# Kernel tuning notes

Hardware: AMD Instinct MI355X
Metric: run time of the kernel (lower is better)

## Reference

```python
import jax, jax.numpy as jnp
import numpy as np

DIM = 128
HEADS = 8
DH = DIM // HEADS
WIN = (4, 4, 4)
TOPK = 4
EPS = 1e-6


def _ln(x, g, b):
    mu = jnp.mean(x, -1, keepdims=True)
    var = jnp.mean((x - mu) ** 2, -1, keepdims=True)
    return (x - mu) * jax.lax.rsqrt(var + EPS) * g + b


def _win3d(x, p1, p2, p3):
    # x: [B,S,H,W,C] -> [B, p1*p2*p3, Ms, Mh, Mw, C]
    B, S, H, W, C = x.shape
    Ms, Mh, Mw = S // p1, H // p2, W // p3
    x = x.reshape(B, p1, Ms, p2, Mh, p3, Mw, C)
    x = x.transpose(0, 1, 3, 5, 2, 4, 6, 7)
    return x.reshape(B, p1 * p2 * p3, Ms, Mh, Mw, C)


def setup_inputs() -> dict:
    key = jax.random.key(0)
    ks = jax.random.split(key, 20)

    def lin(k, din, dout):
        return jax.random.normal(k, (din, dout), jnp.float32) * 0.02

    return {
        "x_in": jax.random.normal(ks[0], (2, 128, 16, 32, 32), jnp.float32),
        "x_g_in": jax.random.normal(ks[1], (2, 128, 8, 16, 16), jnp.float32),
        # Atten (global branch)
        "qkv_w": lin(ks[2], DIM, 3 * DIM), "qkv_b": jnp.zeros((3 * DIM,), jnp.float32),
        "proj_w": lin(ks[3], DIM, DIM), "proj_b": jnp.zeros((DIM,), jnp.float32),
        # shared LayerNorm (self.norm1 is reused everywhere in the original)
        "ln_g": jnp.ones((DIM,), jnp.float32), "ln_b": jnp.zeros((DIM,), jnp.float32),
        # mlp (global branch FFN)
        "mlp_w1": lin(ks[4], DIM, 4 * DIM), "mlp_b1": jnp.zeros((4 * DIM,), jnp.float32),
        "mlp_w2": lin(ks[5], 4 * DIM, DIM), "mlp_b2": jnp.zeros((DIM,), jnp.float32),
        # TopkRouting
        "rq_w": lin(ks[6], DIM, DIM), "rq_b": jnp.zeros((DIM,), jnp.float32),
        "rk_w": lin(ks[7], DIM, DIM), "rk_b": jnp.zeros((DIM,), jnp.float32),
        # fused qkv over concatenated local+gathered-global tokens
        "gqkv_w": lin(ks[8], DIM, 3 * DIM), "gqkv_b": jnp.zeros((3 * DIM,), jnp.float32),
        "wo_w": lin(ks[9], DIM, DIM), "wo_b": jnp.zeros((DIM,), jnp.float32),
        # mlp2 (local branch FFN)
        "mlp2_w1": lin(ks[10], DIM, 4 * DIM), "mlp2_b1": jnp.zeros((4 * DIM,), jnp.float32),
        "mlp2_w2": lin(ks[11], 4 * DIM, DIM), "mlp2_b2": jnp.zeros((DIM,), jnp.float32),
    }


def reference(x_in, x_g_in, qkv_w, qkv_b, proj_w, proj_b, ln_g, ln_b,
              mlp_w1, mlp_b1, mlp_w2, mlp_b2, rq_w, rq_b, rk_w, rk_b,
              gqkv_w, gqkv_b, wo_w, wo_b, mlp2_w1, mlp2_b1, mlp2_w2, mlp2_b2):
    B, C, S, H, W = x_in.shape
    Ms, Mh, Mw = WIN
    p1, p2, p3 = S // Ms, H // Mh, W // Mw  # pads are zero for these shapes
    nw, w3l = p1 * p2 * p3, Ms * Mh * Mw
    scale = DIM ** -0.5  # BiLevelRoutingAttention.scale = dim**-0.5 (not per-head)

    x = jnp.transpose(x_in, (0, 2, 3, 4, 1))  # [B,S,H,W,C]
    shortcut_l = _win3d(x, p1, p2, p3).reshape(B, nw, w3l, C)

    # ---- global branch: full self-attention + FFN ----
    _, _, gS, gH, gW = x_g_in.shape
    gN = gS * gH * gW
    xg = jnp.transpose(x_g_in, (0, 2, 3, 4, 1)).reshape(B, gN, C)
    h = _ln(xg, ln_g, ln_b)
    qkv = (h @ qkv_w + qkv_b).reshape(B, gN, 3, HEADS, DH).transpose(2, 0, 3, 1, 4)
    q, k, v = qkv[0], qkv[1], qkv[2]
    a = jax.nn.softmax(jnp.einsum('bhnd,bhmd->bhnm', q, k) * DH ** -0.5, axis=-1)
    o = jnp.einsum('bhnm,bhmd->bhnd', a, v).transpose(0, 2, 1, 3).reshape(B, gN, C)
    xg = (o @ proj_w + proj_b) + xg
    xg4 = xg.reshape(B, gS, gH, gW, C)
    h = _ln(xg4, ln_g, ln_b)
    xg4 = xg4 + (jax.nn.gelu(h @ mlp_w1 + mlp_b1, approximate=False) @ mlp_w2 + mlp_b2)

    # ---- top-k window routing ----
    swg = _win3d(xg4, p1, p2, p3)  # [B,nw,gMs,gMh,gMw,C]
    w3g = swg.shape[2] * swg.shape[3] * swg.shape[4]
    g_win = swg.mean((2, 3, 4))  # [B,nw,C]
    qh = g_win @ rq_w + rq_b
    kh = g_win @ rk_w + rk_b
    logit = jnp.einsum('bnc,bmc->bnm', qh * scale, kh)
    _tvals, tidx = jax.lax.top_k(logit, TOPK)  # r_weight is computed but unused in the original forward

    # gather top-k global windows' tokens per local window
    gflat = swg.reshape(B, nw, w3g, C)
    gath = jax.vmap(lambda kv, idx: kv[idx])(gflat, tidx)  # [B,nw,topk,w3g,C]
    sc = jnp.concatenate([shortcut_l, gath.reshape(B, nw, TOPK * w3g, C)], axis=2)
    w3 = w3l + TOPK * w3g

    # ---- local+routed attention over concatenated tokens ----
    qkvp = _ln(sc, ln_g, ln_b) @ gqkv_w + gqkv_b
    qp, kp, vp = jnp.split(qkvp, 3, axis=-1)
    qp = qp.reshape(B, nw, w3, HEADS, DH)
    kp = kp.reshape(B, nw, w3, HEADS, DH)
    vp = vp.reshape(B, nw, w3, HEADS, DH)
    aw = jax.nn.softmax(jnp.einsum('bnqhd,bnkhd->bnhqk', qp * scale, kp), axis=-1)
    out = jnp.einsum('bnhqk,bnkhd->bnqhd', aw, vp).reshape(B, nw, w3, C)

    l = out[:, :, :w3l] @ wo_w + wo_b + shortcut_l
    l = l.reshape(B, p1, p2, p3, Ms, Mh, Mw, C).transpose(0, 1, 4, 2, 5, 3, 6, 7).reshape(B, S, H, W, C)
    l = l + (jax.nn.gelu(_ln(l, ln_g, ln_b) @ mlp2_w1 + mlp2_b1, approximate=False) @ mlp2_w2 + mlp2_b2)

    l_out = jnp.transpose(l, (0, 4, 1, 2, 3))
    g_out = jnp.transpose(xg4, (0, 4, 1, 2, 3))
    return (l_out, g_out)
```

## Files before the change

### kernel.cpp

```cpp
#include <hip/hip_runtime.h>
#include <hip/hip_bf16.h>
#include <math.h>

#define BATCH 2
#define CDIM 128
#define SS 16
#define HH_ 32
#define WW_ 32
#define NSP (SS*HH_*WW_)
#define GS 8
#define GH 16
#define GW 16
#define GN (GS*GH*GW)
#define HEADS 8
#define DH 16
#define NW 256
#define W3L 64
#define W3G 8
#define TOPK 4
#define W3 (W3L + TOPK*W3G)
#define LN_EPS 1e-6f
#define ROUTE_SCALE 0.08838834764831845f
#define GATTN_SCALE 0.25f

typedef short bshort8 __attribute__((ext_vector_type(8)));
typedef float f32x4 __attribute__((ext_vector_type(4)));

__device__ __forceinline__ unsigned short f2bf(float f) {
    unsigned int u = __float_as_uint(f);
    unsigned int r = (u + 0x7fffu + ((u >> 16) & 1u)) >> 16;
    return (unsigned short)r;
}
__device__ __forceinline__ float bf2f_lo(unsigned int u) { return __uint_as_float(u << 16); }
__device__ __forceinline__ float bf2f_hi(unsigned int u) { return __uint_as_float(u & 0xffff0000u); }

__device__ __forceinline__ float gelu_exact(float x) {
    return 0.5f * x * (1.0f + erff(x * 0.70710678118654752f));
}

__device__ __forceinline__ float shfl_sum32(float v) {
#pragma unroll
    for (int m = 16; m > 0; m >>= 1) v += __shfl_xor(v, m);
    return v;
}
__device__ __forceinline__ float shfl_sum16(float v) {
#pragma unroll
    for (int m = 8; m > 0; m >>= 1) v += __shfl_xor(v, m);
    return v;
}
__device__ __forceinline__ float shfl_sum8(float v) {
#pragma unroll
    for (int m = 4; m > 0; m >>= 1) v += __shfl_xor(v, m);
    return v;
}

__global__ __launch_bounds__(256) void k_wprep_all(const float* __restrict__ gqkv_w,
        const float* __restrict__ m2_w1, const float* __restrict__ m2_w2,
        const float* __restrict__ proj_w, const float* __restrict__ mlp_w1,
        const float* __restrict__ mlp_w2, const float* __restrict__ wo_w,
        unsigned short* __restrict__ wt, unsigned short* __restrict__ w1t,
        unsigned short* __restrict__ w2t, unsigned short* __restrict__ projt,
        unsigned short* __restrict__ gw1t, unsigned short* __restrict__ gw2t,
        unsigned short* __restrict__ wot) {
    int id = blockIdx.x * 256 + threadIdx.x;
    if (id < 49152) {
        int n = id >> 7, k = id & 127;
        float v = gqkv_w[k * 384 + n];
        if (n < 128) v *= ROUTE_SCALE;
        wt[id] = f2bf(v);
    } else if (id < 114688) {
        int i = id - 49152; int n = i >> 7, k = i & 127;
        w1t[i] = f2bf(m2_w1[k * 512 + n]);
    } else if (id < 180224) {
        int i = id - 114688; int n = i >> 9, k = i & 511;
        w2t[i] = f2bf(m2_w2[k * 128 + n]);
    } else if (id < 196608) {
        int i = id - 180224; int n = i >> 7, k = i & 127;
        projt[i] = f2bf(proj_w[k * 128 + n]);
    } else if (id < 262144) {
        int i = id - 196608; int n = i >> 7, k = i & 127;
        gw1t[i] = f2bf(mlp_w1[k * 512 + n]);
    } else if (id < 327680) {
        int i = id - 262144; int n = i >> 9, k = i & 511;
        gw2t[i] = f2bf(mlp_w2[k * 128 + n]);
    } else {
        int i = id - 327680; int n = i >> 7, k = i & 127;
        wot[i] = f2bf(wo_w[k * 128 + n]);
    }
}

__global__ __launch_bounds__(256) void k_gqkv2(const float* __restrict__ xg_in,
        const float* __restrict__ qkv_w, const float* __restrict__ qkv_b,
        const float* __restrict__ ln_g, const float* __restrict__ ln_b,
        float* __restrict__ xg, unsigned short* __restrict__ qgb,
        unsigned short* __restrict__ kgb, unsigned short* __restrict__ vgtb) {
    int blk = blockIdx.x; int b = blk >> 8; int n0 = (blk & 255) * 8;
    int t = threadIdx.x;
    __shared__ float xs[8][128];
    __shared__ float h[8][128];
    {
        int c = t >> 1, q4 = (t & 1) * 4;
        float4 v = *(const float4*)(xg_in + ((size_t)(b * 128 + c)) * GN + n0 + q4);
        xs[q4 + 0][c] = v.x; xs[q4 + 1][c] = v.y; xs[q4 + 2][c] = v.z; xs[q4 + 3][c] = v.w;
    }
    __syncthreads();
    int j = t >> 5, c4 = (t & 31) * 4;
    float4 v = *(float4*)&xs[j][c4];
    *(float4*)(xg + ((size_t)(b * GN) + n0 + j) * 128 + c4) = v;
    float s1 = shfl_sum32(v.x + v.y + v.z + v.w);
    float mu = s1 * (1.0f / 128.0f);
    float d0 = v.x - mu, d1 = v.y - mu, d2 = v.z - mu, d3 = v.w - mu;
    float s2 = shfl_sum32(d0 * d0 + d1 * d1 + d2 * d2 + d3 * d3);
    float rs = rsqrtf(s2 * (1.0f / 128.0f) + LN_EPS);
    float4 g4 = *(const float4*)(ln_g + c4);
    float4 b4 = *(const float4*)(ln_b + c4);
    float4 hn = { d0 * rs * g4.x + b4.x, d1 * rs * g4.y + b4.y,
                  d2 * rs * g4.z + b4.z, d3 * rs * g4.w + b4.w };
    *(float4*)&h[j][c4] = hn;
    __syncthreads();
    for (int c = t; c < 384; c += 256) {
        float acc[8];
        float bias = qkv_b[c];
#pragma unroll
        for (int jj = 0; jj < 8; jj++) acc[jj] = bias;
        for (int k = 0; k < 128; k++) {
            float w = qkv_w[k * 384 + c];
#pragma unroll
            for (int jj = 0; jj < 8; jj++) acc[jj] = fmaf(h[jj][k], w, acc[jj]);
        }
        int part = c >> 7, head = (c >> 4) & 7, d = c & 15;
        int bh = b * HEADS + head;
        if (part == 0) {
#pragma unroll
            for (int jj = 0; jj < 8; jj++)
                qgb[((size_t)bh * GN + n0 + jj) * DH + d] = f2bf(acc[jj] * GATTN_SCALE);
        } else if (part == 1) {
#pragma unroll
            for (int jj = 0; jj < 8; jj++)
                kgb[((size_t)bh * GN + n0 + jj) * DH + d] = f2bf(acc[jj]);
        } else {
            ushort4 u0, u1;
            u0.x = f2bf(acc[0]); u0.y = f2bf(acc[1]); u0.z = f2bf(acc[2]); u0.w = f2bf(acc[3]);
            u1.x = f2bf(acc[4]); u1.y = f2bf(acc[5]); u1.z = f2bf(acc[6]); u1.w = f2bf(acc[7]);
            unsigned short* dst = vgtb + ((size_t)bh * DH + d) * GN + n0;
            *(ushort4*)dst = u0; *(ushort4*)(dst + 4) = u1;
        }
    }
}

__global__ __launch_bounds__(256) void k_gattn_mfma(const unsigned short* __restrict__ qgb,
        const unsigned short* __restrict__ kgb, const unsigned short* __restrict__ vgtb,
        float* __restrict__ og) {
    int blk = blockIdx.x;
    int bh = blk >> 7; int qt = (blk & 127) << 4;
    int b = bh >> 3, hh = bh & 7;
    int t = threadIdx.x; int w = t >> 6; int lane = t & 63;
    int col = lane & 15, quad = lane >> 4;
    __shared__ __align__(16) unsigned short Pbuf[4 * 16 * 40];
    __shared__ float po[4][64][4];
    __shared__ float pl[4][64][4];

    bshort8 aq = {0, 0, 0, 0, 0, 0, 0, 0};
    if (quad < 2)
        aq = *(const bshort8*)(qgb + ((size_t)bh * GN + qt + col) * DH + quad * 8);

    f32x4 o = {0.f, 0.f, 0.f, 0.f};
    float lsum[4] = {0.f, 0.f, 0.f, 0.f};
    const unsigned short* kb = kgb + (size_t)bh * GN * DH;
    const unsigned short* vb = vgtb + (size_t)bh * DH * GN;
    unsigned short* pb = Pbuf + w * (16 * 40);
    int row0 = quad * 4;
    int kbeg = w * 512;
    for (int kc = kbeg; kc < kbeg + 512; kc += 32) {
        bshort8 bk0 = {0, 0, 0, 0, 0, 0, 0, 0};
        bshort8 bk1 = {0, 0, 0, 0, 0, 0, 0, 0};
        if (quad < 2) {
            bk0 = *(const bshort8*)(kb + (size_t)(kc + col) * DH + quad * 8);
            bk1 = *(const bshort8*)(kb + (size_t)(kc + 16 + col) * DH + quad * 8);
        }
        f32x4 z = {0.f, 0.f, 0.f, 0.f};
        f32x4 s0 = __builtin_amdgcn_mfma_f32_16x16x32_bf16(aq, bk0, z, 0, 0, 0);
        f32x4 s1 = __builtin_amdgcn_mfma_f32_16x16x32_bf16(aq, bk1, z, 0, 0, 0);
        float p0[4], p1[4];
#pragma unroll
        for (int r = 0; r < 4; r++) {
            p0[r] = __expf(s0[r]); p1[r] = __expf(s1[r]);
            lsum[r] += p0[r] + p1[r];
        }
#pragma unroll
        for (int r = 0; r < 4; r++) {
            pb[(row0 + r) * 40 + col] = f2bf(p0[r]);
            pb[(row0 + r) * 40 + 16 + col] = f2bf(p1[r]);
        }
        bshort8 pA = *(const bshort8*)(pb + col * 40 + quad * 8);
        bshort8 bv = *(const bshort8*)(vb + (size_t)col * GN + kc + quad * 8);
        o = __builtin_amdgcn_mfma_f32_16x16x32_bf16(pA, bv, o, 0, 0, 0);
    }
#pragma unroll
    for (int r = 0; r < 4; r++) {
        float v = lsum[r];
        v += __shfl_xor(v, 1); v += __shfl_xor(v, 2);
        v += __shfl_xor(v, 4); v += __shfl_xor(v, 8);
        lsum[r] = v;
    }
#pragma unroll
    for (int r = 0; r < 4; r++) { po[w][lane][r] = o[r]; pl[w][lane][r] = lsum[r]; }
    __syncthreads();
    if (w == 0) {
#pragma unroll
        for (int r = 0; r < 4; r++) {
            float os = po[0][lane][r] + po[1][lane][r] + po[2][lane][r] + po[3][lane][r];
            float ls = pl[0][lane][r] + pl[1][lane][r] + pl[2][lane][r] + pl[3][lane][r];
            og[((size_t)(b * GN) + qt + quad * 4 + r) * 128 + hh * 16 + col] = os / ls;
        }
    }
}

__global__ __launch_bounds__(256) void k_gmlp_mfma(const float* __restrict__ og,
        const float* __restrict__ xg,
        const unsigned short* __restrict__ projt, const float* __restrict__ proj_b,
        const float* __restrict__ ln_g, const float* __restrict__ ln_b,
        const unsigned short* __restrict__ gw1t, const float* __restrict__ b1,
        const unsigned short* __restrict__ gw2t, const float* __restrict__ b2,
        float* __restrict__ xg4, float* __restrict__ gout) {
    int blk = blockIdx.x; int b = blk >> 7; int n0g = (blk & 127) * 16;
    int t = threadIdx.x; int w = t >> 6; int lane = t & 63;
    int l15 = lane & 15, quad = lane >> 4;
    __shared__ __align__(16) unsigned short ao[16 * 136];
// ... 184 lines not shown
    }
}

__global__ __launch_bounds__(256) void k_lnsc_local(const float* __restrict__ x_in,
        const float* __restrict__ ln_g, const float* __restrict__ ln_b,
        unsigned short* __restrict__ lnsc) {
    int blk = blockIdx.x;
    int wt = blk & 1; int hh = (blk >> 1) & 31; int s = (blk >> 6) & 15; int b = blk >> 10;
    int w0 = wt * 16;
    int t = threadIdx.x;
    __shared__ float tile[16][132];
    {
        int c = t >> 1; int wq = (t & 1) * 8;
        const float* src = x_in + (((size_t)(b * 128 + c) * SS + s)) * 1024 + hh * 32 + w0 + wq;
        float4 v0 = *(const float4*)src;
        float4 v1 = *(const float4*)(src + 4);
        tile[wq + 0][c] = v0.x; tile[wq + 1][c] = v0.y; tile[wq + 2][c] = v0.z; tile[wq + 3][c] = v0.w;
        tile[wq + 4][c] = v1.x; tile[wq + 5][c] = v1.y; tile[wq + 6][c] = v1.z; tile[wq + 7][c] = v1.w;
    }
    __syncthreads();
    int w = t >> 4; int j = t & 15;
    float vals[8];
    float s1 = 0.f;
#pragma unroll
    for (int i = 0; i < 8; i++) { vals[i] = tile[w][j * 8 + i]; s1 += vals[i]; }
    s1 = shfl_sum16(s1);
    float mu = s1 * (1.0f / 128.0f);
    float s2 = 0.f;
#pragma unroll
    for (int i = 0; i < 8; i++) { float d = vals[i] - mu; s2 += d * d; }
    s2 = shfl_sum16(s2);
    float rs = rsqrtf(s2 * (1.0f / 128.0f) + LN_EPS);
    float4 g0 = *(const float4*)(ln_g + j * 8);
    float4 g1 = *(const float4*)(ln_g + j * 8 + 4);
    float4 b0 = *(const float4*)(ln_b + j * 8);
    float4 b1 = *(const float4*)(ln_b + j * 8 + 4);
    float gv[8] = { g0.x, g0.y, g0.z, g0.w, g1.x, g1.y, g1.z, g1.w };
    float bv[8] = { b0.x, b0.y, b0.z, b0.w, b1.x, b1.y, b1.z, b1.w };
    int ww = w0 + w;
    int n = (s >> 2) * 64 + (hh >> 2) * 8 + (ww >> 2);
    int slot = (s & 3) * 16 + (hh & 3) * 4 + (ww & 3);
    unsigned short* dst = lnsc + ((size_t)(b * NW + n) * W3 + slot) * 128 + j * 8;
    ushort4 u0, u1;
    u0.x = f2bf((vals[0] - mu) * rs * gv[0] + bv[0]);
    u0.y = f2bf((vals[1] - mu) * rs * gv[1] + bv[1]);
    u0.z = f2bf((vals[2] - mu) * rs * gv[2] + bv[2]);
    u0.w = f2bf((vals[3] - mu) * rs * gv[3] + bv[3]);
    u1.x = f2bf((vals[4] - mu) * rs * gv[4] + bv[4]);
    u1.y = f2bf((vals[5] - mu) * rs * gv[5] + bv[5]);
    u1.z = f2bf((vals[6] - mu) * rs * gv[6] + bv[6]);
    u1.w = f2bf((vals[7] - mu) * rs * gv[7] + bv[7]);
    *(ushort4*)dst = u0;
    *(ushort4*)(dst + 4) = u1;
}

__global__ __launch_bounds__(256) void k_lnsc_gath(const float* __restrict__ xg4,
        const int* __restrict__ tidx,
        const float* __restrict__ ln_g, const float* __restrict__ ln_b,
        unsigned short* __restrict__ lnsc) {
    int blk = blockIdx.x;
    int kk = blk & 3; int wn = blk >> 2;
    int b = wn >> 8;
    int g = tidx[wn * TOPK + kk];
    int gi1 = g >> 6, gi2 = (g >> 3) & 7, gi3 = g & 7;
    int t = threadIdx.x; int j = t >> 5, lj = t & 31;
    int ds = j >> 2, dh = (j >> 1) & 1, dw = j & 1;
    int gi = ((gi1 * 2 + ds) * GH + (gi2 * 2 + dh)) * GW + (gi3 * 2 + dw);
    float4 v = *(const float4*)(xg4 + ((size_t)(b * GN + gi)) * 128 + lj * 4);
    float s1 = shfl_sum32(v.x + v.y + v.z + v.w);
    float mu = s1 * (1.0f / 128.0f);
    float d0 = v.x - mu, d1 = v.y - mu, d2 = v.z - mu, d3 = v.w - mu;
    float s2 = shfl_sum32(d0 * d0 + d1 * d1 + d2 * d2 + d3 * d3);
    float rs = rsqrtf(s2 * (1.0f / 128.0f) + LN_EPS);
    float4 g4 = *(const float4*)(ln_g + lj * 4);
    float4 b4 = *(const float4*)(ln_b + lj * 4);
    ushort4 u;
    u.x = f2bf(d0 * rs * g4.x + b4.x);
    u.y = f2bf(d1 * rs * g4.y + b4.y);
    u.z = f2bf(d2 * rs * g4.z + b4.z);
    u.w = f2bf(d3 * rs * g4.w + b4.w);
    *(ushort4*)(lnsc + ((size_t)wn * W3 + 64 + kk * 8 + j) * 128 + lj * 4) = u;
}

__global__ __launch_bounds__(256) void k_local_mfma(const unsigned short* __restrict__ lnsc,
        const unsigned short* __restrict__ wt, const float* __restrict__ gqkv_b,
        float* __restrict__ aout) {
    int wn = blockIdx.x;
    int t = threadIdx.x; int w = t >> 6; int lane = t & 63;
    int l15 = lane & 15, quad = lane >> 4;
    __shared__ __align__(16) unsigned short Qs[64 * 136];
    __shared__ __align__(16) unsigned short Ks2[96 * 136];
    __shared__ __align__(16) unsigned short Vts[128 * 104];
    __shared__ __align__(16) unsigned short Ps[4][16 * 40];

    const unsigned short* Xb = lnsc + (size_t)wn * W3 * 128;
    f32x4 zero4 = {0.f, 0.f, 0.f, 0.f};

    for (int mt = 0; mt < 4; mt++) {
        bshort8 a[4];
#pragma unroll
        for (int ks = 0; ks < 4; ks++)
            a[ks] = *(const bshort8*)(Xb + (mt * 16 + l15) * 128 + ks * 32 + quad * 8);
#pragma unroll
        for (int which = 0; which < 2; which++) {
            int n0 = (w + which * 4) * 16;
            f32x4 acc = zero4;
#pragma unroll
            for (int ks = 0; ks < 4; ks++) {
                bshort8 bfr = *(const bshort8*)(wt + (n0 + l15) * 128 + ks * 32 + quad * 8);
                acc = __builtin_amdgcn_mfma_f32_16x16x32_bf16(a[ks], bfr, acc, 0, 0, 0);
            }
            float bias = gqkv_b[n0 + l15] * ROUTE_SCALE;
#pragma unroll
            for (int r = 0; r < 4; r++)
                Qs[(mt * 16 + quad * 4 + r) * 136 + n0 + l15] = f2bf(acc[r] + bias);
        }
    }
    for (int mt = 0; mt < 6; mt++) {
        bshort8 a[4];
#pragma unroll
        for (int ks = 0; ks < 4; ks++)
            a[ks] = *(const bshort8*)(Xb + (mt * 16 + l15) * 128 + ks * 32 + quad * 8);
#pragma unroll
        for (int which = 0; which < 2; which++) {
            int nt8 = w + which * 4;
            int n0g = 128 + nt8 * 16;
            f32x4 acc = zero4;
#pragma unroll
            for (int ks = 0; ks < 4; ks++) {
                bshort8 bfr = *(const bshort8*)(wt + (n0g + l15) * 128 + ks * 32 + quad * 8);
                acc = __builtin_amdgcn_mfma_f32_16x16x32_bf16(a[ks], bfr, acc, 0, 0, 0);
            }
            float bias = gqkv_b[n0g + l15];
#pragma unroll
            for (int r = 0; r < 4; r++)
                Ks2[(mt * 16 + quad * 4 + r) * 136 + nt8 * 16 + l15] = f2bf(acc[r] + bias);
        }
    }
    for (int which = 0; which < 2; which++) {
        int mtv = 2 * w + which;
        bshort8 a[4];
#pragma unroll
        for (int ks = 0; ks < 4; ks++)
            a[ks] = *(const bshort8*)(wt + (256 + mtv * 16 + l15) * 128 + ks * 32 + quad * 8);
        float biasr[4];
#pragma unroll
        for (int r = 0; r < 4; r++) biasr[r] = gqkv_b[256 + mtv * 16 + quad * 4 + r];
        for (int ntv = 0; ntv < 6; ntv++) {
            f32x4 acc = zero4;
#pragma unroll
            for (int ks = 0; ks < 4; ks++) {
                bshort8 bfr = *(const bshort8*)(Xb + (ntv * 16 + l15) * 128 + ks * 32 + quad * 8);
                acc = __builtin_amdgcn_mfma_f32_16x16x32_bf16(a[ks], bfr, acc, 0, 0, 0);
            }
#pragma unroll
            for (int r = 0; r < 4; r++)
                Vts[(mtv * 16 + quad * 4 + r) * 104 + ntv * 16 + l15] = f2bf(acc[r] + biasr[r]);
        }
    }
    __syncthreads();

    unsigned short* Pw = &Ps[w][0];
    bshort8 zfrag = {0, 0, 0, 0, 0, 0, 0, 0};
#pragma unroll
    for (int hh2 = 0; hh2 < 2; hh2++) {
        int h = 2 * w + hh2;
        for (int mt = 0; mt < 4; mt++) {
            bshort8 aq = zfrag;
            if (quad < 2)
                aq = *(const bshort8*)(Qs + (mt * 16 + l15) * 136 + h * 16 + quad * 8);
            float rsum[4] = {0.f, 0.f, 0.f, 0.f};
            f32x4 oacc = zero4;
#pragma unroll
            for (int kc = 0; kc < 96; kc += 32) {
#pragma unroll
                for (int sub = 0; sub < 2; sub++) {
                    int nt = (kc >> 4) + sub;
                    bshort8 bk = zfrag;
                    if (quad < 2)
                        bk = *(const bshort8*)(Ks2 + (nt * 16 + l15) * 136 + h * 16 + quad * 8);
                    f32x4 s = __builtin_amdgcn_mfma_f32_16x16x32_bf16(aq, bk, zero4, 0, 0, 0);
#pragma unroll
                    for (int r = 0; r < 4; r++) {
                        float p = __expf(s[r]);
                        rsum[r] += p;
                        Pw[(quad * 4 + r) * 40 + sub * 16 + l15] = f2bf(p);
                    }
                }
                bshort8 ap = *(const bshort8*)(Pw + l15 * 40 + quad * 8);
                bshort8 bv = *(const bshort8*)(Vts + (h * 16 + l15) * 104 + kc + quad * 8);
                oacc = __builtin_amdgcn_mfma_f32_16x16x32_bf16(ap, bv, oacc, 0, 0, 0);
            }
#pragma unroll
            for (int r = 0; r < 4; r++) {
                float v = rsum[r];
                v += __shfl_xor(v, 1); v += __shfl_xor(v, 2);
                v += __shfl_xor(v, 4); v += __shfl_xor(v, 8);
                rsum[r] = v;
            }
#pragma unroll
            for (int r = 0; r < 4; r++)
                aout[((size_t)wn * W3L + mt * 16 + quad * 4 + r) * 128 + h * 16 + l15]
                    = oacc[r] / rsum[r];
        }
    }
}

__global__ __launch_bounds__(256) void k_wo_mfma(const float* __restrict__ aout,
        const unsigned short* __restrict__ wot, const float* __restrict__ wo_b,
        const float* __restrict__ x_in, float* __restrict__ lpre) {
    int blk = blockIdx.x; int T0 = blk * 32;
    int b = T0 >> 14; int sp0 = T0 & 16383;
    int t = threadIdx.x; int w = t >> 6; int lane = t & 63;
    int l15 = lane & 15, quad = lane >> 4;
    __shared__ __align__(16) unsigned short as2[32 * 136];
    __shared__ __align__(16) float xs[32 * 132];
    f32x4 zero4 = {0.f, 0.f, 0.f, 0.f};

    {
        int j = t >> 3, p = t & 7, c0 = p * 16;
        int sp = sp0 + j;
        int s = sp >> 10, hh = (sp >> 5) & 31, ww = sp & 31;
        int n = (s >> 2) * 64 + (hh >> 2) * 8 + (ww >> 2);
        int slot = (s & 3) * 16 + (hh & 3) * 4 + (ww & 3);
        const float* src = aout + (((size_t)(b * NW + n)) * W3L + slot) * 128 + c0;
#pragma unroll
        for (int i4 = 0; i4 < 4; i4++) {
            float4 v = *(const float4*)(src + i4 * 4);
            ushort4 u = { f2bf(v.x), f2bf(v.y), f2bf(v.z), f2bf(v.w) };
            *(ushort4*)&as2[j * 136 + c0 + i4 * 4] = u;
        }
    }
    {
        int c = t >> 1, half = t & 1, j0 = half * 16;
        const float* src = x_in + ((size_t)(b * 128 + c)) * 16384 + sp0 + j0;
#pragma unroll
        for (int i4 = 0; i4 < 4; i4++) {
            float4 v = *(const float4*)(src + i4 * 4);
            xs[(j0 + i4 * 4 + 0) * 132 + c] = v.x;
            xs[(j0 + i4 * 4 + 1) * 132 + c] = v.y;
            xs[(j0 + i4 * 4 + 2) * 132 + c] = v.z;
            xs[(j0 + i4 * 4 + 3) * 132 + c] = v.w;
        }
    }
    __syncthreads();

    bshort8 a[2][4];
#pragma unroll
    for (int mt = 0; mt < 2; mt++)
#pragma unroll
        for (int ks = 0; ks < 4; ks++)
            a[mt][ks] = *(const bshort8*)(as2 + (mt * 16 + l15) * 136 + ks * 32 + quad * 8);
#pragma unroll
    for (int nt = 0; nt < 2; nt++) {
        int n0 = w * 32 + nt * 16;
        f32x4 acc0 = zero4, acc1 = zero4;
#pragma unroll
        for (int ks = 0; ks < 4; ks++) {
            bshort8 bfr = *(const bshort8*)(wot + (n0 + l15) * 128 + ks * 32 + quad * 8);
            acc0 = __builtin_amdgcn_mfma_f32_16x16x32_bf16(a[0][ks], bfr, acc0, 0, 0, 0);
            acc1 = __builtin_amdgcn_mfma_f32_16x16x32_bf16(a[1][ks], bfr, acc1, 0, 0, 0);
        }
        float bias = wo_b[n0 + l15];
#pragma unroll
        for (int r = 0; r < 4; r++) {
            int m0 = quad * 4 + r;
            int m1 = 16 + quad * 4 + r;
            lpre[((size_t)T0 + m0) * 128 + n0 + l15] = acc0[r] + bias + xs[m0 * 132 + n0 + l15];
            lpre[((size_t)T0 + m1) * 128 + n0 + l15] = acc1[r] + bias + xs[m1 * 132 + n0 + l15];
        }
    }
}

__global__ __launch_bounds__(256) void k_mlp2_mfma(const float* __restrict__ lpre,
        const float* __restrict__ ln_g, const float* __restrict__ ln_b,
        const unsigned short* __restrict__ w1t, const float* __restrict__ b1,
        const unsigned short* __restrict__ w2t, const float* __restrict__ b2,
        float* __restrict__ lout) {
    int blk = blockIdx.x;
    int T0 = blk * 32;
    int b = T0 >> 14;
    int sp = T0 & 16383;
    int t = threadIdx.x; int w = t >> 6; int lane = t & 63;
    int l15 = lane & 15, quad = lane >> 4;
    __shared__ __align__(16) unsigned short buf[32 * 520];
    float* of32 = (float*)buf;

// ... 79 lines not shown
            }
        }
    }
    __syncthreads();

#pragma unroll
    for (int mt = 0; mt < 2; mt++) {
#pragma unroll
        for (int nt = 0; nt < 2; nt++) {
            int n0 = w * 32 + nt * 16;
            float bias = b2[n0 + l15];
#pragma unroll
            for (int r = 0; r < 4; r++) {
                int m = mt * 16 + quad * 4 + r;
                float res = lpre[((size_t)T0 + m) * 128 + n0 + l15];
                of32[m * 132 + n0 + l15] = res + acc[mt][nt][r] + bias;
            }
        }
    }
    __syncthreads();

    {
        int c = t >> 1, half = t & 1, j0 = half * 16;
        float* dst = lout + ((size_t)(b * 128 + c)) * NSP + sp + j0;
#pragma unroll
        for (int i4 = 0; i4 < 4; i4++) {
            float4 ov = { of32[(j0 + i4 * 4 + 0) * 132 + c], of32[(j0 + i4 * 4 + 1) * 132 + c],
                          of32[(j0 + i4 * 4 + 2) * 132 + c], of32[(j0 + i4 * 4 + 3) * 132 + c] };
            *(float4*)(dst + i4 * 4) = ov;
        }
    }
}

extern "C" void kernel_launch(void* const* d_in, const int* in_sizes, int n_in,
                              void* d_out, int out_size, void* d_ws, size_t ws_size,
                              hipStream_t stream) {
    const float* x_in   = (const float*)d_in[0];
    const float* xg_in  = (const float*)d_in[1];
    const float* qkv_w  = (const float*)d_in[2];
    const float* qkv_b  = (const float*)d_in[3];
    const float* proj_w = (const float*)d_in[4];
    const float* proj_b = (const float*)d_in[5];
    const float* ln_g   = (const float*)d_in[6];
    const float* ln_b   = (const float*)d_in[7];
    const float* mlp_w1 = (const float*)d_in[8];
    const float* mlp_b1 = (const float*)d_in[9];
    const float* mlp_w2 = (const float*)d_in[10];
    const float* mlp_b2 = (const float*)d_in[11];
    const float* rq_w   = (const float*)d_in[12];
    const float* rq_b   = (const float*)d_in[13];
    const float* rk_w   = (const float*)d_in[14];
    const float* rk_b   = (const float*)d_in[15];
    const float* gqkv_w = (const float*)d_in[16];
    const float* gqkv_b = (const float*)d_in[17];
    const float* wo_w   = (const float*)d_in[18];
    const float* wo_b   = (const float*)d_in[19];
    const float* m2_w1  = (const float*)d_in[20];
    const float* m2_b1  = (const float*)d_in[21];
    const float* m2_w2  = (const float*)d_in[22];
    const float* m2_b2  = (const float*)d_in[23];

    float* out = (float*)d_out;
    float* ws  = (float*)d_ws;

    float* xg4 = ws;
    float* xg  = ws + 524288;
    unsigned short* qgb  = (unsigned short*)(ws + 1048576);
    unsigned short* kgb  = (unsigned short*)(ws + 1310720);
    unsigned short* vgtb = (unsigned short*)(ws + 1572864);
    float* og  = ws + 1835008;
    float* qh  = ws + 2359296;
    float* kh  = ws + 2424832;
    int*   tidx = (int*)(ws + 2490368);
    unsigned short* lnsc = (unsigned short*)(ws + 2492416);
    float* aout = ws + 2492416 + 3145728;
    float* lpre = ws + 9832448;
    unsigned short* wt   = (unsigned short*)(ws + 14026752);
    unsigned short* w1t  = (unsigned short*)(ws + 14051328);
    unsigned short* w2t  = (unsigned short*)(ws + 14084096);
    unsigned short* projt = (unsigned short*)(ws + 14116864);
    unsigned short* gw1t  = (unsigned short*)(ws + 14125056);
    unsigned short* gw2t  = (unsigned short*)(ws + 14157824);
    unsigned short* wot   = (unsigned short*)(ws + 14190592);

    const size_t L_OUT = (size_t)BATCH * CDIM * NSP;
    float* gout = out + L_OUT;

    hipLaunchKernelGGL(k_wprep_all, dim3(1344), dim3(256), 0, stream,
                       gqkv_w, m2_w1, m2_w2, proj_w, mlp_w1, mlp_w2, wo_w,
                       wt, w1t, w2t, projt, gw1t, gw2t, wot);
    hipLaunchKernelGGL(k_gqkv2, dim3(512), dim3(256), 0, stream,
                       xg_in, qkv_w, qkv_b, ln_g, ln_b, xg, qgb, kgb, vgtb);
    hipLaunchKernelGGL(k_gattn_mfma, dim3(2048), dim3(256), 0, stream, qgb, kgb, vgtb, og);
    hipLaunchKernelGGL(k_gmlp_mfma, dim3(256), dim3(256), 0, stream,
                       og, xg, projt, proj_b, ln_g, ln_b, gw1t, mlp_b1, gw2t, mlp_b2,
                       xg4, gout);
    hipLaunchKernelGGL(k_routing_qk, dim3(512), dim3(128), 0, stream,
                       xg4, rq_w, rq_b, rk_w, rk_b, qh, kh);
    hipLaunchKernelGGL(k_topk, dim3(512), dim3(256), 0, stream, qh, kh, tidx);
    hipLaunchKernelGGL(k_lnsc_local, dim3(2048), dim3(256), 0, stream,
                       x_in, ln_g, ln_b, lnsc);
    hipLaunchKernelGGL(k_lnsc_gath, dim3(2048), dim3(256), 0, stream,
                       xg4, tidx, ln_g, ln_b, lnsc);
    hipLaunchKernelGGL(k_local_mfma, dim3(512), dim3(256), 0, stream,
                       lnsc, wt, gqkv_b, aout);
    hipLaunchKernelGGL(k_wo_mfma, dim3(1024), dim3(256), 0, stream,
                       aout, wot, wo_b, x_in, lpre);
    hipLaunchKernelGGL(k_mlp2_mfma, dim3(1024), dim3(256), 0, stream,
                       lpre, ln_g, ln_b, w1t, m2_b1, w2t, m2_b2, out);
}
```

Measured before the change: 307.3 us.

## Split local attention kernel across head pairs to quadruple grid size

New measurement: 328.6 us. 1.07x slower.

```diff
diff --git a/kernel.cpp b/kernel.cpp
--- a/kernel.cpp
+++ b/kernel.cpp
@@ -494,127 +494,121 @@
     *(ushort4*)(lnsc + ((size_t)wn * W3 + 64 + kk * 8 + j) * 128 + lj * 4) = u;
 }
 
-__global__ __launch_bounds__(256) void k_local_mfma(const unsigned short* __restrict__ lnsc,
+__global__ __launch_bounds__(256) void k_local_mfma2(const unsigned short* __restrict__ lnsc,
         const unsigned short* __restrict__ wt, const float* __restrict__ gqkv_b,
         float* __restrict__ aout) {
-    int wn = blockIdx.x;
+    int blk = blockIdx.x;
+    int hp = blk & 3; int wn = blk >> 2;
     int t = threadIdx.x; int w = t >> 6; int lane = t & 63;
     int l15 = lane & 15, quad = lane >> 4;
-    __shared__ __align__(16) unsigned short Qs[64 * 136];
-    __shared__ __align__(16) unsigned short Ks2[96 * 136];
-    __shared__ __align__(16) unsigned short Vts[128 * 104];
+    __shared__ __align__(16) unsigned short Qs[64 * 40];
+    __shared__ __align__(16) unsigned short Ks[96 * 40];
+    __shared__ __align__(16) unsigned short Vts[32 * 104];
     __shared__ __align__(16) unsigned short Ps[4][16 * 40];
 
     const unsigned short* Xb = lnsc + (size_t)wn * W3 * 128;
     f32x4 zero4 = {0.f, 0.f, 0.f, 0.f};
 
-    for (int mt = 0; mt < 4; mt++) {
+    {
+        int mt = w;
         bshort8 a[4];
 #pragma unroll
         for (int ks = 0; ks < 4; ks++)
             a[ks] = *(const bshort8*)(Xb + (mt * 16 + l15) * 128 + ks * 32 + quad * 8);
 #pragma unroll
-        for (int which = 0; which < 2; which++) {
-            int n0 = (w + which * 4) * 16;
+        for (int nt = 0; nt < 2; nt++) {
+            int ng = hp * 32 + nt * 16;
             f32x4 acc = zero4;
 #pragma unroll
             for (int ks = 0; ks < 4; ks++) {
-                bshort8 bfr = *(const bshort8*)(wt + (n0 + l15) * 128 + ks * 32 + quad * 8);
+                bshort8 bfr = *(const bshort8*)(wt + (ng + l15) * 128 + ks * 32 + quad * 8);
                 acc = __builtin_amdgcn_mfma_f32_16x16x32_bf16(a[ks], bfr, acc, 0, 0, 0);
             }
-            float bias = gqkv_b[n0 + l15] * ROUTE_SCALE;
+            float bias = gqkv_b[ng + l15] * ROUTE_SCALE;
 #pragma unroll
             for (int r = 0; r < 4; r++)
-                Qs[(mt * 16 + quad * 4 + r) * 136 + n0 + l15] = f2bf(acc[r] + bias);
-        }
-    }
-    for (int mt = 0; mt < 6; mt++) {
+                Qs[(mt * 16 + quad * 4 + r) * 40 + nt * 16 + l15] = f2bf(acc[r] + bias);
+        }
+    }
+    for (int idx = w; idx < 12; idx += 4) {
+        int mt = idx >> 1, nt = idx & 1;
         bshort8 a[4];
 #pragma unroll
         for (int ks = 0; ks < 4; ks++)
             a[ks] = *(const bshort8*)(Xb + (mt * 16 + l15) * 128 + ks * 32 + quad * 8);
-#pragma unroll
-        for (int which = 0; which < 2; which++) {
-            int nt8 = w + which * 4;
-            int n0g = 128 + nt8 * 16;
-            f32x4 acc = zero4;
-#pragma unroll
-            for (int ks = 0; ks < 4; ks++) {
-                bshort8 bfr = *(const bshort8*)(wt + (n0g + l15) * 128 + ks * 32 + quad * 8);
-                acc = __builtin_amdgcn_mfma_f32_16x16x32_bf16(a[ks], bfr, acc, 0, 0, 0);
-            }
-            float bias = gqkv_b[n0g + l15];
-#pragma unroll
-            for (int r = 0; r < 4; r++)
-                Ks2[(mt * 16 + quad * 4 + r) * 136 + nt8 * 16 + l15] = f2bf(acc[r] + bias);
-        }
-    }
-    for (int which = 0; which < 2; which++) {
-        int mtv = 2 * w + which;
+        int ng = 128 + hp * 32 + nt * 16;
+        f32x4 acc = zero4;
+#pragma unroll
+        for (int ks = 0; ks < 4; ks++) {
+            bshort8 bfr = *(const bshort8*)(wt + (ng + l15) * 128 + ks * 32 + quad * 8);
+            acc = __builtin_amdgcn_mfma_f32_16x16x32_bf16(a[ks], bfr, acc, 0, 0, 0);
+        }
+        float bias = gqkv_b[ng + l15];
+#pragma unroll
+        for (int r = 0; r < 4; r++)
+            Ks[(mt * 16 + quad * 4 + r) * 40 + nt * 16 + l15] = f2bf(acc[r] + bias);
+    }
+    for (int idx = w; idx < 12; idx += 4) {
+        int mtv = idx / 6, ntv = idx % 6;
+        int vg = 256 + hp * 32 + mtv * 16;
         bshort8 a[4];
 #pragma unroll
         for (int ks = 0; ks < 4; ks++)
-            a[ks] = *(const bshort8*)(wt + (256 + mtv * 16 + l15) * 128 + ks * 32 + quad * 8);
-        float biasr[4];
-#pragma unroll
-        for (int r = 0; r < 4; r++) biasr[r] = gqkv_b[256 + mtv * 16 + quad * 4 + r];
-        for (int ntv = 0; ntv < 6; ntv++) {
-            f32x4 acc = zero4;
-#pragma unroll
-            for (int ks = 0; ks < 4; ks++) {
-                bshort8 bfr = *(const bshort8*)(Xb + (ntv * 16 + l15) * 128 + ks * 32 + quad * 8);
-                acc = __builtin_amdgcn_mfma_f32_16x16x32_bf16(a[ks], bfr, acc, 0, 0, 0);
-            }
-#pragma unroll
-            for (int r = 0; r < 4; r++)
-                Vts[(mtv * 16 + quad * 4 + r) * 104 + ntv * 16 + l15] = f2bf(acc[r] + biasr[r]);
+            a[ks] = *(const bshort8*)(wt + (vg + l15) * 128 + ks * 32 + quad * 8);
+        f32x4 acc = zero4;
+#pragma unroll
+        for (int ks = 0; ks < 4; ks++) {
+            bshort8 bfr = *(const bshort8*)(Xb + (ntv * 16 + l15) * 128 + ks * 32 + quad * 8);
+            acc = __builtin_amdgcn_mfma_f32_16x16x32_bf16(a[ks], bfr, acc, 0, 0, 0);
+        }
+#pragma unroll
+        for (int r = 0; r < 4; r++) {
+            float bias = gqkv_b[vg + quad * 4 + r];
+            Vts[(mtv * 16 + quad * 4 + r) * 104 + ntv * 16 + l15] = f2bf(acc[r] + bias);
         }
     }
     __syncthreads();
 
     unsigned short* Pw = &Ps[w][0];
     bshort8 zfrag = {0, 0, 0, 0, 0, 0, 0, 0};
-#pragma unroll
-    for (int hh2 = 0; hh2 < 2; hh2++) {
-        int h = 2 * w + hh2;
-        for (int mt = 0; mt < 4; mt++) {
-            bshort8 aq = zfrag;
-            if (quad < 2)
-                aq = *(const bshort8*)(Qs + (mt * 16 + l15) * 136 + h * 16 + quad * 8);
-            float rsum[4] = {0.f, 0.f, 0.f, 0.f};
-            f32x4 oacc = zero4;
-#pragma unroll
-            for (int kc = 0; kc < 96; kc += 32) {
-#pragma unroll
-                for (int sub = 0; sub < 2; sub++) {
-                    int nt = (kc >> 4) + sub;
-                    bshort8 bk = zfrag;
-                    if (quad < 2)
-                        bk = *(const bshort8*)(Ks2 + (nt * 16 + l15) * 136 + h * 16 + quad * 8);
-                    f32x4 s = __builtin_amdgcn_mfma_f32_16x16x32_bf16(aq, bk, zero4, 0, 0, 0);
-#pragma unroll
-                    for (int r = 0; r < 4; r++) {
-                        float p = __expf(s[r]);
-                        rsum[r] += p;
-                        Pw[(quad * 4 + r) * 40 + sub * 16 + l15] = f2bf(p);
-                    }
+    for (int c = w; c < 8; c += 4) {
+        int hloc = c >> 2, mt = c & 3;
+        bshort8 aq = zfrag;
+        if (quad < 2)
+            aq = *(const bshort8*)(Qs + (mt * 16 + l15) * 40 + hloc * 16 + quad * 8);
+        float rsum[4] = {0.f, 0.f, 0.f, 0.f};
+        f32x4 oacc = zero4;
+#pragma unroll
+        for (int kc = 0; kc < 96; kc += 32) {
+#pragma unroll
+            for (int sub = 0; sub < 2; sub++) {
+                int nt = (kc >> 4) + sub;
+                bshort8 bk = zfrag;
+                if (quad < 2)
+                    bk = *(const bshort8*)(Ks + (nt * 16 + l15) * 40 + hloc * 16 + quad * 8);
+                f32x4 s = __builtin_amdgcn_mfma_f32_16x16x32_bf16(aq, bk, zero4, 0, 0, 0);
+#pragma unroll
+                for (int r = 0; r < 4; r++) {
+                    float p = __expf(s[r]);
+                    rsum[r] += p;
+                    Pw[(quad * 4 + r) * 40 + sub * 16 + l15] = f2bf(p);
                 }
-                bshort8 ap = *(const bshort8*)(Pw + l15 * 40 + quad * 8);
-                bshort8 bv = *(const bshort8*)(Vts + (h * 16 + l15) * 104 + kc + quad * 8);
-                oacc = __builtin_amdgcn_mfma_f32_16x16x32_bf16(ap, bv, oacc, 0, 0, 0);
-            }
-#pragma unroll
-            for (int r = 0; r < 4; r++) {
-                float v = rsum[r];
-                v += __shfl_xor(v, 1); v += __shfl_xor(v, 2);
-                v += __shfl_xor(v, 4); v += __shfl_xor(v, 8);
-                rsum[r] = v;
-            }
-#pragma unroll
-            for (int r = 0; r < 4; r++)
-                aout[((size_t)wn * W3L + mt * 16 + quad * 4 + r) * 128 + h * 16 + l15]
-                    = oacc[r] / rsum[r];
-        }
+            }
+            bshort8 ap = *(const bshort8*)(Pw + l15 * 40 + quad * 8);
+            bshort8 bv = *(const bshort8*)(Vts + (hloc * 16 + l15) * 104 + kc + quad * 8);
+            oacc = __builtin_amdgcn_mfma_f32_16x16x32_bf16(ap, bv, oacc, 0, 0, 0);
+        }
+#pragma unroll
+        for (int r = 0; r < 4; r++) {
+            float v = rsum[r];
+            v += __shfl_xor(v, 1); v += __shfl_xor(v, 2);
+            v += __shfl_xor(v, 4); v += __shfl_xor(v, 8);
+            rsum[r] = v;
+        }
+#pragma unroll
+        for (int r = 0; r < 4; r++)
+            aout[((size_t)wn * W3L + mt * 16 + quad * 4 + r) * 128 + hp * 32 + hloc * 16 + l15]
+                = oacc[r] / rsum[r];
     }
 }
 
@@ -880,7 +874,7 @@
                        x_in, ln_g, ln_b, lnsc);
     hipLaunchKernelGGL(k_lnsc_gath, dim3(2048), dim3(256), 0, stream,
                        xg4, tidx, ln_g, ln_b, lnsc);
-    hipLaunchKernelGGL(k_local_mfma, dim3(512), dim3(256), 0, stream,
+    hipLaunchKernelGGL(k_local_mfma2, dim3(2048), dim3(256), 0, stream,
                        lnsc, wt, gqkv_b, aout);
     hipLaunchKernelGGL(k_wo_mfma, dim3(1024), dim3(256), 0, stream,
                        aout, wot, wo_b, x_in, lpre);
```

## Stage window tokens in swizzled LDS and keep Q fragments in registers

Applied to the files above, without the earlier changes.

Measured after the change: 368.7 us. 20.0% more time.

```diff
diff --git a/kernel.cpp b/kernel.cpp
--- a/kernel.cpp
+++ b/kernel.cpp
@@ -52,6 +52,11 @@
 #pragma unroll
     for (int m = 4; m > 0; m >>= 1) v += __shfl_xor(v, m);
     return v;
+}
+
+__device__ __forceinline__ bshort8 lds_swz(const unsigned short* S, int row, int g) {
+    int sg = g ^ (row & 7);
+    return *(const bshort8*)&S[row * 128 + sg * 8];
 }
 
 __global__ __launch_bounds__(256) void k_wprep_all(const float* __restrict__ gqkv_w,
@@ -494,45 +499,58 @@
     *(ushort4*)(lnsc + ((size_t)wn * W3 + 64 + kk * 8 + j) * 128 + lj * 4) = u;
 }
 
-__global__ __launch_bounds__(256) void k_local_mfma(const unsigned short* __restrict__ lnsc,
+__global__ __launch_bounds__(256) void k_local_mfma3(const unsigned short* __restrict__ lnsc,
         const unsigned short* __restrict__ wt, const float* __restrict__ gqkv_b,
         float* __restrict__ aout) {
     int wn = blockIdx.x;
     int t = threadIdx.x; int w = t >> 6; int lane = t & 63;
     int l15 = lane & 15, quad = lane >> 4;
-    __shared__ __align__(16) unsigned short Qs[64 * 136];
-    __shared__ __align__(16) unsigned short Ks2[96 * 136];
+    __shared__ __align__(16) unsigned short Xs[96 * 128];
+    __shared__ __align__(16) unsigned short Ks[96 * 128];
     __shared__ __align__(16) unsigned short Vts[128 * 104];
     __shared__ __align__(16) unsigned short Ps[4][16 * 40];
 
     const unsigned short* Xb = lnsc + (size_t)wn * W3 * 128;
     f32x4 zero4 = {0.f, 0.f, 0.f, 0.f};
-
-    for (int mt = 0; mt < 4; mt++) {
-        bshort8 a[4];
-#pragma unroll
-        for (int ks = 0; ks < 4; ks++)
-            a[ks] = *(const bshort8*)(Xb + (mt * 16 + l15) * 128 + ks * 32 + quad * 8);
-#pragma unroll
-        for (int which = 0; which < 2; which++) {
-            int n0 = (w + which * 4) * 16;
+    bshort8 zfrag = {0, 0, 0, 0, 0, 0, 0, 0};
+    unsigned short* Pw = &Ps[w][0];
+
+#pragma unroll
+    for (int i = 0; i < 6; i++) {
+        int e = t + 256 * i;
+        int row = e >> 4, g = e & 15;
+        int sg = g ^ (row & 7);
+        *(bshort8*)&Xs[row * 128 + sg * 8] = *(const bshort8*)&Xb[row * 128 + g * 8];
+    }
+    __syncthreads();
+
+    bshort8 qfrag[2][4];
+#pragma unroll
+    for (int hh2 = 0; hh2 < 2; hh2++) {
+        int h = 2 * w + hh2;
+        for (int mt = 0; mt < 4; mt++) {
             f32x4 acc = zero4;
 #pragma unroll
             for (int ks = 0; ks < 4; ks++) {
-                bshort8 bfr = *(const bshort8*)(wt + (n0 + l15) * 128 + ks * 32 + quad * 8);
-                acc = __builtin_amdgcn_mfma_f32_16x16x32_bf16(a[ks], bfr, acc, 0, 0, 0);
-            }
-            float bias = gqkv_b[n0 + l15] * ROUTE_SCALE;
+                bshort8 a = lds_swz(Xs, mt * 16 + l15, ks * 4 + quad);
+                bshort8 bfr = *(const bshort8*)(wt + (h * 16 + l15) * 128 + ks * 32 + quad * 8);
+                acc = __builtin_amdgcn_mfma_f32_16x16x32_bf16(a, bfr, acc, 0, 0, 0);
+            }
+            float bias = gqkv_b[h * 16 + l15] * ROUTE_SCALE;
 #pragma unroll
             for (int r = 0; r < 4; r++)
-                Qs[(mt * 16 + quad * 4 + r) * 136 + n0 + l15] = f2bf(acc[r] + bias);
-        }
-    }
+                Pw[(quad * 4 + r) * 40 + l15] = f2bf(acc[r] + bias);
+            bshort8 aq = zfrag;
+            if (quad < 2) aq = *(const bshort8*)(Pw + l15 * 40 + quad * 8);
+            qfrag[hh2][mt] = aq;
+        }
+    }
+
     for (int mt = 0; mt < 6; mt++) {
         bshort8 a[4];
 #pragma unroll
         for (int ks = 0; ks < 4; ks++)
-            a[ks] = *(const bshort8*)(Xb + (mt * 16 + l15) * 128 + ks * 32 + quad * 8);
+            a[ks] = lds_swz(Xs, mt * 16 + l15, ks * 4 + quad);
 #pragma unroll
         for (int which = 0; which < 2; which++) {
             int nt8 = w + which * 4;
@@ -544,9 +562,13 @@
                 acc = __builtin_amdgcn_mfma_f32_16x16x32_bf16(a[ks], bfr, acc, 0, 0, 0);
             }
             float bias = gqkv_b[n0g + l15];
-#pragma unroll
-            for (int r = 0; r < 4; r++)
-                Ks2[(mt * 16 + quad * 4 + r) * 136 + nt8 * 16 + l15] = f2bf(acc[r] + bias);
+            int col = nt8 * 16 + l15;
+            int gcol = col >> 3, e = col & 7;
+#pragma unroll
+            for (int r = 0; r < 4; r++) {
+                int row = mt * 16 + quad * 4 + r;
+                Ks[row * 128 + ((gcol ^ (row & 7)) << 3) + e] = f2bf(acc[r] + bias);
+            }
         }
     }
     for (int which = 0; which < 2; which++) {
@@ -562,7 +584,7 @@
             f32x4 acc = zero4;
 #pragma unroll
             for (int ks = 0; ks < 4; ks++) {
-                bshort8 bfr = *(const bshort8*)(Xb + (ntv * 16 + l15) * 128 + ks * 32 + quad * 8);
+                bshort8 bfr = lds_swz(Xs, ntv * 16 + l15, ks * 4 + quad);
                 acc = __builtin_amdgcn_mfma_f32_16x16x32_bf16(a[ks], bfr, acc, 0, 0, 0);
             }
 #pragma unroll
@@ -572,15 +594,11 @@
     }
     __syncthreads();
 
-    unsigned short* Pw = &Ps[w][0];
-    bshort8 zfrag = {0, 0, 0, 0, 0, 0, 0, 0};
 #pragma unroll
     for (int hh2 = 0; hh2 < 2; hh2++) {
         int h = 2 * w + hh2;
         for (int mt = 0; mt < 4; mt++) {
-            bshort8 aq = zfrag;
-            if (quad < 2)
-                aq = *(const bshort8*)(Qs + (mt * 16 + l15) * 136 + h * 16 + quad * 8);
+            bshort8 aq = qfrag[hh2][mt];
             float rsum[4] = {0.f, 0.f, 0.f, 0.f};
             f32x4 oacc = zero4;
 #pragma unroll
@@ -589,8 +607,11 @@
                 for (int sub = 0; sub < 2; sub++) {
                     int nt = (kc >> 4) + sub;
                     bshort8 bk = zfrag;
-                    if (quad < 2)
-                        bk = *(const bshort8*)(Ks2 + (nt * 16 + l15) * 136 + h * 16 + quad * 8);
+                    if (quad < 2) {
+                        int row = nt * 16 + l15;
+                        int sg = (h * 2 + quad) ^ (row & 7);
+                        bk = *(const bshort8*)&Ks[row * 128 + sg * 8];
+                    }
                     f32x4 s = __builtin_amdgcn_mfma_f32_16x16x32_bf16(aq, bk, zero4, 0, 0, 0);
 #pragma unroll
                     for (int r = 0; r < 4; r++) {
@@ -880,7 +901,7 @@
                        x_in, ln_g, ln_b, lnsc);
     hipLaunchKernelGGL(k_lnsc_gath, dim3(2048), dim3(256), 0, stream,
                        xg4, tidx, ln_g, ln_b, lnsc);
-    hipLaunchKernelGGL(k_local_mfma, dim3(512), dim3(256), 0, stream,
+    hipLaunchKernelGGL(k_local_mfma3, dim3(512), dim3(256), 0, stream,
                        lnsc, wt, gqkv_b, aout);
     hipLaunchKernelGGL(k_wo_mfma, dim3(1024), dim3(256), 0, stream,
                        aout, wot, wo_b, x_in, lpre);
```

## Compute global QKV projection with bf16 MFMA and pre-transposed scaled weights

Applied to the files above, without the earlier changes.

New measurement: 288.7 us. 1.06x faster.

```diff
diff --git a/kernel.cpp b/kernel.cpp
--- a/kernel.cpp
+++ b/kernel.cpp
@@ -31,13 +31,9 @@
     unsigned int r = (u + 0x7fffu + ((u >> 16) & 1u)) >> 16;
     return (unsigned short)r;
 }
-__device__ __forceinline__ float bf2f_lo(unsigned int u) { return __uint_as_float(u << 16); }
-__device__ __forceinline__ float bf2f_hi(unsigned int u) { return __uint_as_float(u & 0xffff0000u); }
-
 __device__ __forceinline__ float gelu_exact(float x) {
     return 0.5f * x * (1.0f + erff(x * 0.70710678118654752f));
 }
-
 __device__ __forceinline__ float shfl_sum32(float v) {
 #pragma unroll
     for (int m = 16; m > 0; m >>= 1) v += __shfl_xor(v, m);
@@ -58,10 +54,11 @@
         const float* __restrict__ m2_w1, const float* __restrict__ m2_w2,
         const float* __restrict__ proj_w, const float* __restrict__ mlp_w1,
         const float* __restrict__ mlp_w2, const float* __restrict__ wo_w,
+        const float* __restrict__ qkv_w,
         unsigned short* __restrict__ wt, unsigned short* __restrict__ w1t,
         unsigned short* __restrict__ w2t, unsigned short* __restrict__ projt,
         unsigned short* __restrict__ gw1t, unsigned short* __restrict__ gw2t,
-        unsigned short* __restrict__ wot) {
+        unsigned short* __restrict__ wot, unsigned short* __restrict__ qkvt) {
     int id = blockIdx.x * 256 + threadIdx.x;
     if (id < 49152) {
         int n = id >> 7, k = id & 127;
@@ -83,67 +80,107 @@
     } else if (id < 327680) {
         int i = id - 262144; int n = i >> 9, k = i & 511;
         gw2t[i] = f2bf(mlp_w2[k * 128 + n]);
-    } else {
+    } else if (id < 344064) {
         int i = id - 327680; int n = i >> 7, k = i & 127;
         wot[i] = f2bf(wo_w[k * 128 + n]);
-    }
-}
-
-__global__ __launch_bounds__(256) void k_gqkv2(const float* __restrict__ xg_in,
-        const float* __restrict__ qkv_w, const float* __restrict__ qkv_b,
+    } else {
+        int i = id - 344064; int n = i >> 7, k = i & 127;
+        float v = qkv_w[k * 384 + n];
+        if (n < 128) v *= GATTN_SCALE;
+        qkvt[i] = f2bf(v);
+    }
+}
+
+__global__ __launch_bounds__(256) void k_gqkv_mfma(const float* __restrict__ xg_in,
+        const unsigned short* __restrict__ qkvt, const float* __restrict__ qkv_b,
         const float* __restrict__ ln_g, const float* __restrict__ ln_b,
         float* __restrict__ xg, unsigned short* __restrict__ qgb,
         unsigned short* __restrict__ kgb, unsigned short* __restrict__ vgtb) {
-    int blk = blockIdx.x; int b = blk >> 8; int n0 = (blk & 255) * 8;
-    int t = threadIdx.x;
-    __shared__ float xs[8][128];
-    __shared__ float h[8][128];
-    {
-        int c = t >> 1, q4 = (t & 1) * 4;
-        float4 v = *(const float4*)(xg_in + ((size_t)(b * 128 + c)) * GN + n0 + q4);
-        xs[q4 + 0][c] = v.x; xs[q4 + 1][c] = v.y; xs[q4 + 2][c] = v.z; xs[q4 + 3][c] = v.w;
-    }
-    __syncthreads();
-    int j = t >> 5, c4 = (t & 31) * 4;
-    float4 v = *(float4*)&xs[j][c4];
-    *(float4*)(xg + ((size_t)(b * GN) + n0 + j) * 128 + c4) = v;
-    float s1 = shfl_sum32(v.x + v.y + v.z + v.w);
-    float mu = s1 * (1.0f / 128.0f);
-    float d0 = v.x - mu, d1 = v.y - mu, d2 = v.z - mu, d3 = v.w - mu;
-    float s2 = shfl_sum32(d0 * d0 + d1 * d1 + d2 * d2 + d3 * d3);
-    float rs = rsqrtf(s2 * (1.0f / 128.0f) + LN_EPS);
-    float4 g4 = *(const float4*)(ln_g + c4);
-    float4 b4 = *(const float4*)(ln_b + c4);
-    float4 hn = { d0 * rs * g4.x + b4.x, d1 * rs * g4.y + b4.y,
-                  d2 * rs * g4.z + b4.z, d3 * rs * g4.w + b4.w };
-    *(float4*)&h[j][c4] = hn;
-    __syncthreads();
-    for (int c = t; c < 384; c += 256) {
-        float acc[8];
-        float bias = qkv_b[c];
-#pragma unroll
-        for (int jj = 0; jj < 8; jj++) acc[jj] = bias;
-        for (int k = 0; k < 128; k++) {
-            float w = qkv_w[k * 384 + c];
-#pragma unroll
-            for (int jj = 0; jj < 8; jj++) acc[jj] = fmaf(h[jj][k], w, acc[jj]);
-        }
-        int part = c >> 7, head = (c >> 4) & 7, d = c & 15;
-        int bh = b * HEADS + head;
-        if (part == 0) {
-#pragma unroll
-            for (int jj = 0; jj < 8; jj++)
-                qgb[((size_t)bh * GN + n0 + jj) * DH + d] = f2bf(acc[jj] * GATTN_SCALE);
-        } else if (part == 1) {
-#pragma unroll
-            for (int jj = 0; jj < 8; jj++)
-                kgb[((size_t)bh * GN + n0 + jj) * DH + d] = f2bf(acc[jj]);
-        } else {
-            ushort4 u0, u1;
-            u0.x = f2bf(acc[0]); u0.y = f2bf(acc[1]); u0.z = f2bf(acc[2]); u0.w = f2bf(acc[3]);
-            u1.x = f2bf(acc[4]); u1.y = f2bf(acc[5]); u1.z = f2bf(acc[6]); u1.w = f2bf(acc[7]);
-            unsigned short* dst = vgtb + ((size_t)bh * DH + d) * GN + n0;
-            *(ushort4*)dst = u0; *(ushort4*)(dst + 4) = u1;
+    int blk = blockIdx.x; int b = blk >> 7; int n0 = (blk & 127) * 16;
+    int t = threadIdx.x; int w = t >> 6; int lane = t & 63;
+    int l15 = lane & 15, quad = lane >> 4;
+    __shared__ __align__(16) float xs[16 * 132];
+    __shared__ __align__(16) unsigned short h[16 * 136];
+    f32x4 zero4 = {0.f, 0.f, 0.f, 0.f};
+
+    {
+        int c = t >> 1, j0 = (t & 1) * 8;
+        const float* src = xg_in + ((size_t)(b * 128 + c)) * GN + n0 + j0;
+        float4 v0 = *(const float4*)src;
+        float4 v1 = *(const float4*)(src + 4);
+        xs[(j0 + 0) * 132 + c] = v0.x; xs[(j0 + 1) * 132 + c] = v0.y;
+        xs[(j0 + 2) * 132 + c] = v0.z; xs[(j0 + 3) * 132 + c] = v0.w;
+        xs[(j0 + 4) * 132 + c] = v1.x; xs[(j0 + 5) * 132 + c] = v1.y;
+        xs[(j0 + 6) * 132 + c] = v1.z; xs[(j0 + 7) * 132 + c] = v1.w;
+    }
+    __syncthreads();
+    {
+        int j = t >> 4, p = t & 15, c0 = p * 8;
+        float vv[8]; float s1 = 0.f;
+#pragma unroll
+        for (int i = 0; i < 8; i++) { vv[i] = xs[j * 132 + c0 + i]; s1 += vv[i]; }
+        s1 = shfl_sum16(s1);
+        float mu = s1 * (1.0f / 128.0f);
+        float s2 = 0.f;
+#pragma unroll
+        for (int i = 0; i < 8; i++) { float d = vv[i] - mu; s2 += d * d; }
+        s2 = shfl_sum16(s2);
+        float rs = rsqrtf(s2 * (1.0f / 128.0f) + LN_EPS);
+        float* dst = xg + ((size_t)(b * GN) + n0 + j) * 128 + c0;
+        *(float4*)dst = *(float4*)&vv[0];
+        *(float4*)(dst + 4) = *(float4*)&vv[4];
+        unsigned short hb[8];
+#pragma unroll
+        for (int i4 = 0; i4 < 2; i4++) {
+            float4 g4 = *(const float4*)(ln_g + c0 + i4 * 4);
+            float4 b4 = *(const float4*)(ln_b + c0 + i4 * 4);
+            hb[i4 * 4 + 0] = f2bf((vv[i4 * 4 + 0] - mu) * rs * g4.x + b4.x);
+            hb[i4 * 4 + 1] = f2bf((vv[i4 * 4 + 1] - mu) * rs * g4.y + b4.y);
+            hb[i4 * 4 + 2] = f2bf((vv[i4 * 4 + 2] - mu) * rs * g4.z + b4.z);
+            hb[i4 * 4 + 3] = f2bf((vv[i4 * 4 + 3] - mu) * rs * g4.w + b4.w);
+        }
+        *(ushort4*)&h[j * 136 + c0] = *(ushort4*)&hb[0];
+        *(ushort4*)&h[j * 136 + c0 + 4] = *(ushort4*)&hb[4];
+    }
+    __syncthreads();
+
+    bshort8 a[4];
+#pragma unroll
+    for (int ks = 0; ks < 4; ks++)
+        a[ks] = *(const bshort8*)(h + l15 * 136 + ks * 32 + quad * 8);
+    int bh_base = b * HEADS;
+#pragma unroll
+    for (int part = 0; part < 2; part++) {
+#pragma unroll
+        for (int which = 0; which < 2; which++) {
+            int nt = 2 * w + which;
+            int ncol = part * 128 + nt * 16;
+            f32x4 acc = zero4;
+#pragma unroll
+            for (int ks = 0; ks < 4; ks++) {
+                bshort8 bfr = *(const bshort8*)(qkvt + (size_t)(ncol + l15) * 128 + ks * 32 + quad * 8);
+                acc = __builtin_amdgcn_mfma_f32_16x16x32_bf16(a[ks], bfr, acc, 0, 0, 0);
+            }
+            float bias = qkv_b[ncol + l15] * (part == 0 ? GATTN_SCALE : 1.f);
+            unsigned short* dst = (part == 0) ? qgb : kgb;
+#pragma unroll
+            for (int r = 0; r < 4; r++)
+                dst[((size_t)(bh_base + nt) * GN + n0 + quad * 4 + r) * DH + l15] = f2bf(acc[r] + bias);
+        }
+    }
+#pragma unroll
+    for (int which = 0; which < 2; which++) {
+        int mtv = 2 * w + which;
+        f32x4 acc = zero4;
+#pragma unroll
+        for (int ks = 0; ks < 4; ks++) {
+            bshort8 aw = *(const bshort8*)(qkvt + (size_t)(256 + mtv * 16 + l15) * 128 + ks * 32 + quad * 8);
+            acc = __builtin_amdgcn_mfma_f32_16x16x32_bf16(aw, a[ks], acc, 0, 0, 0);
+        }
+#pragma unroll
+        for (int r = 0; r < 4; r++) {
+            float bias = qkv_b[256 + mtv * 16 + quad * 4 + r];
+            vgtb[((size_t)(bh_base + mtv) * DH + quad * 4 + r) * GN + n0 + l15] = f2bf(acc[r] + bias);
         }
     }
 }
@@ -860,15 +897,16 @@
     unsigned short* gw1t  = (unsigned short*)(ws + 14125056);
     unsigned short* gw2t  = (unsigned short*)(ws + 14157824);
     unsigned short* wot   = (unsigned short*)(ws + 14190592);
+    unsigned short* qkvt  = (unsigned short*)(ws + 14198784);
 
     const size_t L_OUT = (size_t)BATCH * CDIM * NSP;
     float* gout = out + L_OUT;
 
-    hipLaunchKernelGGL(k_wprep_all, dim3(1344), dim3(256), 0, stream,
-                       gqkv_w, m2_w1, m2_w2, proj_w, mlp_w1, mlp_w2, wo_w,
-                       wt, w1t, w2t, projt, gw1t, gw2t, wot);
-    hipLaunchKernelGGL(k_gqkv2, dim3(512), dim3(256), 0, stream,
-                       xg_in, qkv_w, qkv_b, ln_g, ln_b, xg, qgb, kgb, vgtb);
+    hipLaunchKernelGGL(k_wprep_all, dim3(1536), dim3(256), 0, stream,
+                       gqkv_w, m2_w1, m2_w2, proj_w, mlp_w1, mlp_w2, wo_w, qkv_w,
+                       wt, w1t, w2t, projt, gw1t, gw2t, wot, qkvt);
+    hipLaunchKernelGGL(k_gqkv_mfma, dim3(256), dim3(256), 0, stream,
+                       xg_in, qkvt, qkv_b, ln_g, ln_b, xg, qgb, kgb, vgtb);
     hipLaunchKernelGGL(k_gattn_mfma, dim3(2048), dim3(256), 0, stream, qgb, kgb, vgtb, og);
     hipLaunchKernelGGL(k_gmlp_mfma, dim3(256), dim3(256), 0, stream,
                        og, xg, projt, proj_b, ln_g, ln_b, gw1t, mlp_b1, gw2t, mlp_b2,
```
